# Optimization experiments

Measured on AMD Instinct MI355X. Metric: run time of the kernel, lower is better.

The kernel has to match this reference:

```python
import jax, jax.numpy as jnp
import numpy as np

N_SOURCE = 100000
N_TARGET = 4096
DEG = 800                      # edges per target (uniform)
N_EDGES = N_TARGET * DEG       # 3,276,800
SOURCE_DIM = 512
EMBED_DIM = 32
TARGET_DIM = 16


def setup_inputs() -> dict:
    key = jax.random.key(0)
    k1, k2, k3, k4, k5 = jax.random.split(key, 5)
    source_feat = jax.random.normal(k1, (N_SOURCE, SOURCE_DIM), dtype=jnp.float32)
    embed = jax.random.normal(k2, (SOURCE_DIM, EMBED_DIM), dtype=jnp.float32)
    weight = jax.random.normal(k3, (EMBED_DIM, TARGET_DIM), dtype=jnp.float32)
    # edges sorted by target; range_list[i] = [start, end) of target i's edge block
    src = jax.random.randint(k4, (N_EDGES,), 0, N_SOURCE, dtype=jnp.int64)
    tgt = jnp.repeat(jnp.arange(N_TARGET, dtype=jnp.int64), DEG)
    edge_index = jnp.stack([src, tgt], axis=0)
    starts = jnp.arange(N_TARGET, dtype=jnp.int64) * DEG
    range_list = jnp.stack([starts, starts + DEG], axis=1)
    x_norm = jax.random.uniform(k5, (N_SOURCE,), dtype=jnp.float32) + 0.5
    return {"source_feat": source_feat, "embed": embed, "weight": weight,
            "edge_index": edge_index, "range_list": range_list, "x_norm": x_norm}


def reference(source_feat, embed, weight, edge_index, range_list, x_norm):
    # dense embed GEMM + row normalization
    x = jnp.matmul(source_feat, embed)              # [N_SOURCE, EMBED_DIM]
    x = x / x_norm[:, None]
    # hierarchical conv: gather source rows, mean-aggregate per target segment
    tmp = x[edge_index[0]]                           # [N_EDGES, EMBED_DIM]
    agg = jax.ops.segment_sum(tmp, edge_index[1], num_segments=N_TARGET)
    deg = (range_list[:, 1] - range_list[:, 0]).astype(x.dtype)
    out = agg / jnp.maximum(deg, 1.0)[:, None]       # [N_TARGET, EMBED_DIM]
    out = jnp.matmul(out, weight)                    # [N_TARGET, TARGET_DIM]
    return out
```

## Files before the change

kernel.cpp:

```cpp
#include <hip/hip_runtime.h>
#include <hip/hip_bf16.h>

#define N_SOURCE   100000
#define N_TARGET   4096
#define SOURCE_DIM 512
#define EMBED_DIM  32
#define TARGET_DIM 16
#define NTILES     ((N_SOURCE + 15) / 16)

typedef __attribute__((ext_vector_type(8))) short short8;
typedef __attribute__((ext_vector_type(4))) float f32x4;

static __device__ __forceinline__ ushort f2bf(float f) {
    __hip_bfloat16 h = __float2bfloat16(f);
    return *(ushort*)&h;
}

__global__ __launch_bounds__(256)
void k_embed_weight(const float* __restrict__ embed,
                    const float* __restrict__ weight,
                    ushort* __restrict__ Mt) {
    __shared__ float wlds[EMBED_DIM * TARGET_DIM];
    int tid = threadIdx.x;
    for (int i = tid; i < EMBED_DIM * TARGET_DIM; i += 256)
        wlds[i] = weight[i];
    __syncthreads();

    int idx = blockIdx.x * 256 + tid;
    if (idx < SOURCE_DIM * TARGET_DIM) {
        int k = idx >> 4;
        int o = idx & 15;
        float s = 0.f;
        #pragma unroll
        for (int j = 0; j < EMBED_DIM; ++j)
            s += embed[k * EMBED_DIM + j] * wlds[j * TARGET_DIM + o];
        Mt[o * SOURCE_DIM + k] = f2bf(s);
    }
}

__global__ __launch_bounds__(256, 2)
void k_gemm_y(const float*  __restrict__ A,
              const float*  __restrict__ xnorm,
              const ushort* __restrict__ Mt,
              ushort*       __restrict__ y) {
    __shared__ ushort Bl[SOURCE_DIM * TARGET_DIM];
    int tid  = threadIdx.x;
    int wave = tid >> 6;
    int lane = tid & 63;
    int n    = lane & 15;
    int g    = lane >> 4;

    #pragma unroll
    for (int i = 0; i < 4; ++i) {
        int c  = tid + 256 * i;
        int nn = c & 15;
        int kg = c >> 4;
        int kk = kg >> 2;
        int gg = kg & 3;
        *(uint4*)&Bl[c * 8] =
            *(const uint4*)(Mt + nn * SOURCE_DIM + kk * 32 + gg * 8);
    }
    __syncthreads();

    int tile = blockIdx.x * 4 + wave;
    if (tile < NTILES) {
        int row0 = tile * 16;

        int lr = lane >> 2;
        int q  = lane & 3;
        const float* Aload = A + (size_t)(row0 + lr) * SOURCE_DIM + q * 4;

        f32x4 buf[32];
        #pragma unroll
        for (int kk = 0; kk < 16; ++kk) {
            buf[2 * kk]     = *(const f32x4*)(Aload + kk * 32);
            buf[2 * kk + 1] = *(const f32x4*)(Aload + kk * 32 + 16);
        }

        int sA = (n << 2) | ((2 * g) & 3);
        int sB = (n << 2) | ((2 * g + 1) & 3);
        bool hi = g >= 2;

        const ushort* Bll = Bl + lane * 8;

        f32x4 acc = {0.f, 0.f, 0.f, 0.f};
        #pragma unroll
        for (int kk = 0; kk < 16; ++kk) {
            f32x4 a0 = buf[2 * kk];
            f32x4 a1 = buf[2 * kk + 1];

            uint u00 = (uint)f2bf(a0[0]) | ((uint)f2bf(a0[1]) << 16);
            uint u01 = (uint)f2bf(a0[2]) | ((uint)f2bf(a0[3]) << 16);
            uint u10 = (uint)f2bf(a1[0]) | ((uint)f2bf(a1[1]) << 16);
            uint u11 = (uint)f2bf(a1[2]) | ((uint)f2bf(a1[3]) << 16);

            uint e0 = (uint)__shfl((int)u00, sA);
            uint e1 = (uint)__shfl((int)u01, sA);
            uint e2 = (uint)__shfl((int)u00, sB);
            uint e3 = (uint)__shfl((int)u01, sB);
            uint f0 = (uint)__shfl((int)u10, sA);
            uint f1 = (uint)__shfl((int)u11, sA);
            uint f2 = (uint)__shfl((int)u10, sB);
            uint f3 = (uint)__shfl((int)u11, sB);

            union { short8 s; uint u[4]; } af;
            af.u[0] = hi ? f0 : e0;
            af.u[1] = hi ? f1 : e1;
            af.u[2] = hi ? f2 : e2;
            af.u[3] = hi ? f3 : e3;

            short8 bf = *(const short8*)(Bll + kk * 512);
            acc = __builtin_amdgcn_mfma_f32_16x16x32_bf16(af.s, bf, acc, 0, 0, 0);
        }

        int m0 = g * 4;
        float4 xn = *(const float4*)(xnorm + row0 + m0);
        const float xr[4] = {xn.x, xn.y, xn.z, xn.w};
        #pragma unroll
        for (int r = 0; r < 4; ++r)
            y[(size_t)(row0 + m0 + r) * TARGET_DIM + n] = f2bf(acc[r] / xr[r]);
    }
}

__global__ __launch_bounds__(256)
void k_gather_mean(const ushort* __restrict__ y,
                   const int*    __restrict__ src,
                   const int*    __restrict__ rl,
                   float* __restrict__ out) {
    int t     = blockIdx.x;
    int tid   = threadIdx.x;
    int start = rl[2 * t];
    int end   = rl[2 * t + 1];

    int slot = tid >> 1;
    int sub  = tid & 1;

    float a[8];
    #pragma unroll
    for (int i = 0; i < 8; ++i) a[i] = 0.f;

    for (int base = start + slot * 4; base < end; base += 512) {
        int rem = end - base;
        int id[4];
        if (rem >= 4) {
            int4 qd = *(const int4*)(src + base);
            id[0] = qd.x; id[1] = qd.y; id[2] = qd.z; id[3] = qd.w;
        } else {
            #pragma unroll
            for (int j = 0; j < 4; ++j) id[j] = (j < rem) ? src[base + j] : 0;
        }
        #pragma unroll
        for (int j = 0; j < 4; ++j) {
            if (j < rem) {
                uint4 v = *(const uint4*)(y + (size_t)id[j] * TARGET_DIM + sub * 8);
                const uint w[4] = {v.x, v.y, v.z, v.w};
                #pragma unroll
                for (int i = 0; i < 4; ++i) {
                    uint lo = w[i] << 16;
                    uint hiw = w[i] & 0xffff0000u;
                    a[2 * i]     += *(float*)&lo;
                    a[2 * i + 1] += *(float*)&hiw;
                }
            }
        }
    }

    #pragma unroll
    for (int m = 2; m <= 32; m <<= 1) {
        #pragma unroll
        for (int i = 0; i < 8; ++i) a[i] += __shfl_xor(a[i], m);
    }

    __shared__ float red[4][16];
    int wid  = tid >> 6;
    int lane = tid & 63;
    if (lane < 2) {
        #pragma unroll
        for (int i = 0; i < 8; ++i) red[wid][lane * 8 + i] = a[i];
    }
    __syncthreads();

    if (tid < TARGET_DIM) {
        float s = red[0][tid] + red[1][tid] + red[2][tid] + red[3][tid];
        float deg = (float)(end - start);
        deg = deg > 1.f ? deg : 1.f;
        out[t * TARGET_DIM + tid] = s / deg;
    }
}

extern "C" void kernel_launch(void* const* d_in, const int* in_sizes, int n_in,
                              void* d_out, int out_size, void* d_ws, size_t ws_size,
                              hipStream_t stream) {
    const float* source_feat = (const float*)d_in[0];
    const float* embed       = (const float*)d_in[1];
    const float* weight      = (const float*)d_in[2];
    const int*   edge_src    = (const int*)d_in[3];
    const int*   range_list  = (const int*)d_in[4];
    const float* x_norm      = (const float*)d_in[5];

    float*  out = (float*)d_out;
    ushort* Mt  = (ushort*)d_ws;
    ushort* y   = (ushort*)((char*)d_ws + 16384);

    k_embed_weight<<<32, 256, 0, stream>>>(embed, weight, Mt);

    int nblk = (NTILES + 3) / 4;
    k_gemm_y<<<nblk, 256, 0, stream>>>(source_feat, x_norm, Mt, y);

    k_gather_mean<<<N_TARGET, 256, 0, stream>>>(y, edge_src, range_list, out);
}
```

Before: 65.48 us.

## Fuse embed*weight precompute into GEMM kernel, redundantly per block

Drops the separate embed*weight kernel launch. Each GEMM block now computes its own bf16 copy of the 512x16 combined matrix directly into LDS, and the A-tile loads are issued before that computation so their latency overlaps it. This removes one launch and the global round trip for Mt. In exchange every one of roughly 1563 blocks redoes 512x16x32 FMAs and reads all of embed, which adds a lot of redundant ALU and L2 traffic.

```diff
diff --git a/kernel.cpp b/kernel.cpp
--- a/kernel.cpp
+++ b/kernel.cpp
@@ -16,32 +16,11 @@
     return *(ushort*)&h;
 }
 
-__global__ __launch_bounds__(256)
-void k_embed_weight(const float* __restrict__ embed,
-                    const float* __restrict__ weight,
-                    ushort* __restrict__ Mt) {
-    __shared__ float wlds[EMBED_DIM * TARGET_DIM];
-    int tid = threadIdx.x;
-    for (int i = tid; i < EMBED_DIM * TARGET_DIM; i += 256)
-        wlds[i] = weight[i];
-    __syncthreads();
-
-    int idx = blockIdx.x * 256 + tid;
-    if (idx < SOURCE_DIM * TARGET_DIM) {
-        int k = idx >> 4;
-        int o = idx & 15;
-        float s = 0.f;
-        #pragma unroll
-        for (int j = 0; j < EMBED_DIM; ++j)
-            s += embed[k * EMBED_DIM + j] * wlds[j * TARGET_DIM + o];
-        Mt[o * SOURCE_DIM + k] = f2bf(s);
-    }
-}
-
 __global__ __launch_bounds__(256, 2)
 void k_gemm_y(const float*  __restrict__ A,
               const float*  __restrict__ xnorm,
-              const ushort* __restrict__ Mt,
+              const float*  __restrict__ embed,
+              const float*  __restrict__ weight,
               ushort*       __restrict__ y) {
     __shared__ ushort Bl[SOURCE_DIM * TARGET_DIM];
     int tid  = threadIdx.x;
@@ -50,33 +29,49 @@
     int n    = lane & 15;
     int g    = lane >> 4;
 
+    int tile  = blockIdx.x * 4 + wave;
+    int tilec = tile < NTILES ? tile : NTILES - 1;
+    int row0  = tilec * 16;
+    int lr = lane >> 2;
+    int q  = lane & 3;
+    const float* Aload = A + (size_t)(row0 + lr) * SOURCE_DIM + q * 4;
+
+    f32x4 buf[32];
+    #pragma unroll
+    for (int kk = 0; kk < 16; ++kk) {
+        buf[2 * kk]     = *(const f32x4*)(Aload + kk * 32);
+        buf[2 * kk + 1] = *(const f32x4*)(Aload + kk * 32 + 16);
+    }
+
+    int nn = tid & 15;
+    float wcol[EMBED_DIM];
+    #pragma unroll
+    for (int j = 0; j < EMBED_DIM; ++j)
+        wcol[j] = weight[j * TARGET_DIM + nn];
+
     #pragma unroll
     for (int i = 0; i < 4; ++i) {
         int c  = tid + 256 * i;
-        int nn = c & 15;
         int kg = c >> 4;
-        int kk = kg >> 2;
-        int gg = kg & 3;
-        *(uint4*)&Bl[c * 8] =
-            *(const uint4*)(Mt + nn * SOURCE_DIM + kk * 32 + gg * 8);
+        int k0 = (kg >> 2) * 32 + (kg & 3) * 8;
+        uint d[4];
+        #pragma unroll
+        for (int p = 0; p < 4; ++p) {
+            const float* e0 = embed + (size_t)(k0 + 2 * p)     * EMBED_DIM;
+            const float* e1 = embed + (size_t)(k0 + 2 * p + 1) * EMBED_DIM;
+            float s0 = 0.f, s1 = 0.f;
+            #pragma unroll
+            for (int j = 0; j < EMBED_DIM; ++j) {
+                s0 += e0[j] * wcol[j];
+                s1 += e1[j] * wcol[j];
+            }
+            d[p] = (uint)f2bf(s0) | ((uint)f2bf(s1) << 16);
+        }
+        *(uint4*)&Bl[c * 8] = make_uint4(d[0], d[1], d[2], d[3]);
     }
     __syncthreads();
 
-    int tile = blockIdx.x * 4 + wave;
     if (tile < NTILES) {
-        int row0 = tile * 16;
-
-        int lr = lane >> 2;
-        int q  = lane & 3;
-        const float* Aload = A + (size_t)(row0 + lr) * SOURCE_DIM + q * 4;
-
-        f32x4 buf[32];
-        #pragma unroll
-        for (int kk = 0; kk < 16; ++kk) {
-            buf[2 * kk]     = *(const f32x4*)(Aload + kk * 32);
-            buf[2 * kk + 1] = *(const f32x4*)(Aload + kk * 32 + 16);
-        }
-
         int sA = (n << 2) | ((2 * g) & 3);
         int sB = (n << 2) | ((2 * g + 1) & 3);
         bool hi = g >= 2;
@@ -199,13 +194,10 @@
     const float* x_norm      = (const float*)d_in[5];
 
     float*  out = (float*)d_out;
-    ushort* Mt  = (ushort*)d_ws;
-    ushort* y   = (ushort*)((char*)d_ws + 16384);
-
-    k_embed_weight<<<32, 256, 0, stream>>>(embed, weight, Mt);
+    ushort* y   = (ushort*)d_ws;
 
     int nblk = (NTILES + 3) / 4;
-    k_gemm_y<<<nblk, 256, 0, stream>>>(source_feat, x_norm, Mt, y);
+    k_gemm_y<<<nblk, 256, 0, stream>>>(source_feat, x_norm, embed, weight, y);
 
     k_gather_mean<<<N_TARGET, 256, 0, stream>>>(y, edge_src, range_list, out);
 }
```

New measurement: 110.6 us. 1.69x slower.
